# Performance work log

Measured on AMD Instinct MI355X. Metric: run time of the kernel, lower is better.

The kernel has to match this reference:

```python
import jax, jax.numpy as jnp
import numpy as np

SCALING = 32.0 / 16.0  # alpha / r

def setup_inputs() -> dict:
    key = jax.random.key(0)
    k1, k2, k3, k4 = jax.random.split(key, 4)
    B_, S, D_in, D_out, R = 4, 2048, 4096, 4096, 16
    x = jax.random.normal(k1, (B_, S, D_in), dtype=jnp.float32)
    W_base = jax.random.normal(k2, (D_out, D_in), dtype=jnp.float32) * 0.02
    b_base = jax.random.normal(k3, (D_out,), dtype=jnp.float32) * 0.02
    A = jax.random.normal(k4, (R, D_in), dtype=jnp.float32) * 0.02
    B = jnp.zeros((D_out, R), dtype=jnp.float32)  # lora_B init to zeros
    return {"x": x, "W_base": W_base, "b_base": b_base, "A": A, "B": B}

def reference(x, W_base, b_base, A, B):
    # base linear (stands in for dequantized 4-bit matmul): [B,S,Din] @ [Din,Dout]
    out = jnp.einsum('bsd,od->bso', x, W_base) + b_base
    # LoRA path: B(A(x)) * scaling, dropout=0 -> identity
    xa = jnp.einsum('bsd,rd->bsr', x, A)        # [B,S,r]
    delta = jnp.einsum('bsr,or->bso', xa, B)    # [B,S,Dout]
    return out + delta * SCALING
```

## Files before the change

### kernel.cpp

```cpp
#include <hip/hip_runtime.h>


typedef __attribute__((ext_vector_type(4))) float f32x4;
typedef __attribute__((ext_vector_type(8))) short bf16x8;

__device__ __forceinline__ unsigned short f2bf(float f) {
    unsigned u = __builtin_bit_cast(unsigned, f);
    unsigned r = u + 0x7fffu + ((u >> 16) & 1u);
    return (unsigned short)(r >> 16);
}

__device__ __forceinline__ void gload_lds16(const void* g, void* l) {
    __builtin_amdgcn_global_load_lds(
        (const __attribute__((address_space(1))) void*)g,
        (__attribute__((address_space(3))) void*)l, 16, 0, 0);
}

__global__ __launch_bounds__(256) void cast_x_kernel(
    const float* __restrict__ x, unsigned short* __restrict__ xb, int n8)
{
    int stride = gridDim.x * blockDim.x;
    for (int i = blockIdx.x * blockDim.x + threadIdx.x; i < n8; i += stride) {
        size_t base = (size_t)i * 8;
        float4 f0 = *(const float4*)&x[base];
        float4 f1 = *(const float4*)&x[base + 4];
        ushort4 o0, o1;
        o0.x = f2bf(f0.x); o0.y = f2bf(f0.y); o0.z = f2bf(f0.z); o0.w = f2bf(f0.w);
        o1.x = f2bf(f1.x); o1.y = f2bf(f1.y); o1.z = f2bf(f1.z); o1.w = f2bf(f1.w);
        *(ushort4*)&xb[base]     = o0;
        *(ushort4*)&xb[base + 4] = o1;
    }
}

__global__ __launch_bounds__(256) void prep_w_kernel(
    const float* __restrict__ W, const float* __restrict__ A,
    const float* __restrict__ Bl, unsigned short* __restrict__ wb,
    int K, float scale)
{
    __shared__ float Bs[16][16];
    const int t = threadIdx.x;
    const int n0 = blockIdx.y * 16;
    const int k0 = blockIdx.x * 256;
    {
        int nl = t >> 4, r = t & 15;
        Bs[nl][r] = Bl[(size_t)(n0 + nl) * 16 + r];
    }
    __syncthreads();

    const int lane = t & 63;
    const int wv = t >> 6;
    const int k = k0 + lane * 4;

    float4 av[16];
#pragma unroll
    for (int r = 0; r < 16; ++r)
        av[r] = *(const float4*)&A[(size_t)r * K + k];

#pragma unroll
    for (int j = 0; j < 4; ++j) {
        const int nl = wv * 4 + j;
        const int n = n0 + nl;
        float4 w = *(const float4*)&W[(size_t)n * K + k];
        float d0 = 0.f, d1 = 0.f, d2 = 0.f, d3 = 0.f;
#pragma unroll
        for (int r = 0; r < 16; ++r) {
            float b = Bs[nl][r];
            d0 += b * av[r].x; d1 += b * av[r].y;
            d2 += b * av[r].z; d3 += b * av[r].w;
        }
        ushort4 o;
        o.x = f2bf(w.x + scale * d0);
        o.y = f2bf(w.y + scale * d1);
        o.z = f2bf(w.z + scale * d2);
        o.w = f2bf(w.w + scale * d3);
        *(ushort4*)&wb[(size_t)n * K + k] = o;
    }
}


#define SETPRIO(p) __builtin_amdgcn_s_setprio(p)
#define BARRIER()  __builtin_amdgcn_s_barrier()
#define LGKM0()    do { asm volatile("s_waitcnt lgkmcnt(0)" ::: "memory"); \
                        __builtin_amdgcn_sched_barrier(0); } while (0)

__global__ __launch_bounds__(512, 2) void gemm256_kernel(
    const unsigned short* __restrict__ Xb, const unsigned short* __restrict__ Wb,
    const float* __restrict__ bias, float* __restrict__ out,
    int M, int N, int K)
{
    __shared__ __align__(16) unsigned short lds[2][2][2][8192];

    const int NT = K / 64;
    const int ntn = N / 256;
    int bid = blockIdx.x;
    {
        int per = gridDim.x >> 3;
        bid = (bid & 7) * per + (bid >> 3);
    }
    const int tm = bid / ntn, tn = bid % ntn;

    const int t = threadIdx.x;
    const int lane = t & 63, wave = t >> 6;
    const int wr = wave >> 2;
    const int wc = wave & 3;

    const int srow = t >> 3;
    const int scol = ((t & 7) * 8) ^ (((t >> 3) & 7) << 3);
    unsigned gA[2][2], gB[2][2];
#pragma unroll
    for (int h = 0; h < 2; ++h)
#pragma unroll
        for (int i = 0; i < 2; ++i) {
            gA[h][i] = (unsigned)((tm * 256 + h * 128 + i * 64 + srow) * K + scol);
            gB[h][i] = (unsigned)((tn * 256 + h * 128 + i * 64 + srow) * K + scol);
        }

#define ST_A(buf, h, i, kt)                                                     \
    gload_lds16(Xb + gA[h][i] + (kt) * 64,                                      \
                &lds[buf][0][h][(i) * 4096 + wave * 512]);
#define ST_B(buf, h, i, kt)                                                     \
    gload_lds16(Wb + gB[h][i] + (kt) * 64,                                      \
                &lds[buf][1][h][(i) * 4096 + wave * 512]);

    const int fr = lane & 15;
    const int hi16 = ((lane >> 4) & 3) * 16;
    const int bsw = (fr & 7) << 4;
    const int lo0 = hi16 ^ bsw;
    const int lo1 = (64 + hi16) ^ bsw;

    f32x4 acc[8][4] = {};

#pragma unroll
    for (int h = 0; h < 2; ++h)
#pragma unroll
        for (int i = 0; i < 2; ++i) { ST_A(0, h, i, 0) ST_B(0, h, i, 0) }
#pragma unroll
    for (int h = 0; h < 2; ++h)
#pragma unroll
        for (int i = 0; i < 2; ++i) { ST_A(1, h, i, 1) }
    asm volatile("s_waitcnt vmcnt(4)" ::: "memory");
    BARRIER();

#define MFMA_Q(m0, n0)                                                          \
    _Pragma("unroll") for (int mi = m0; mi < m0 + 4; ++mi)                      \
    _Pragma("unroll") for (int ni = n0; ni < n0 + 2; ++ni)                      \
    _Pragma("unroll") for (int kk = 0; kk < 2; ++kk)                            \
        acc[mi][ni] = __builtin_amdgcn_mfma_f32_16x16x32_bf16(                  \
            a[mi][kk], b[ni][kk], acc[mi][ni], 0, 0, 0);

    for (int kt = 0; kt < NT; ++kt) {
        const int cur = kt & 1;
        const char* pA = (const char*)&lds[cur][0][wr][0];
        const char* pB = (const char*)&lds[cur][1][wc >> 1][0];
        const int bro = (wc & 1) * 64;
        const bool stB = (kt + 1 < NT);
        const bool stA = (kt + 2 < NT);

        bf16x8 a[8][2], b[4][2];

#pragma unroll
        for (int mi = 0; mi < 4; ++mi) {
            a[mi][0] = *(const bf16x8*)(pA + (mi * 16 + fr) * 128 + lo0);
            a[mi][1] = *(const bf16x8*)(pA + (mi * 16 + fr) * 128 + lo1);
        }
#pragma unroll
        for (int ni = 0; ni < 2; ++ni) {
            b[ni][0] = *(const bf16x8*)(pB + (bro + ni * 16 + fr) * 128 + lo0);
            b[ni][1] = *(const bf16x8*)(pB + (bro + ni * 16 + fr) * 128 + lo1);
        }
        if (stB) { ST_B(cur ^ 1, 0, 0, kt + 1) ST_B(cur ^ 1, 0, 1, kt + 1) }
        BARRIER();
        LGKM0();
        SETPRIO(1);
        MFMA_Q(0, 0)
        SETPRIO(0);
        BARRIER();

#pragma unroll
        for (int mi = 4; mi < 8; ++mi) {
            a[mi][0] = *(const bf16x8*)(pA + (mi * 16 + fr) * 128 + lo0);
            a[mi][1] = *(const bf16x8*)(pA + (mi * 16 + fr) * 128 + lo1);
        }
        if (stB) { ST_B(cur ^ 1, 1, 0, kt + 1) ST_B(cur ^ 1, 1, 1, kt + 1) }
        BARRIER();
        LGKM0();
        SETPRIO(1);
        MFMA_Q(4, 0)
        SETPRIO(0);
        BARRIER();

#pragma unroll
        for (int ni = 2; ni < 4; ++ni) {
            b[ni][0] = *(const bf16x8*)(pB + (bro + ni * 16 + fr) * 128 + lo0);
            b[ni][1] = *(const bf16x8*)(pB + (bro + ni * 16 + fr) * 128 + lo1);
        }
        if (stA) { ST_A(cur, 0, 0, kt + 2) ST_A(cur, 0, 1, kt + 2) }
        BARRIER();
        LGKM0();
        SETPRIO(1);
        MFMA_Q(0, 2)
        SETPRIO(0);
        BARRIER();

        if (stA) { ST_A(cur, 1, 0, kt + 2) ST_A(cur, 1, 1, kt + 2) }
        BARRIER();
        SETPRIO(1);
        MFMA_Q(4, 2)
        SETPRIO(0);
        if (stA) {
            asm volatile("s_waitcnt vmcnt(4)" ::: "memory");
        } else {
            asm volatile("s_waitcnt vmcnt(0)" ::: "memory");
        }
        BARRIER();
    }

    const int row0 = tm * 256 + wr * 128 + (lane >> 4) * 4;
    const int col0 = tn * 256 + wc * 64;
#pragma unroll
    for (int ni = 0; ni < 4; ++ni) {
        const int col = col0 + ni * 16 + fr;
        const float bv = bias[col];
#pragma unroll
        for (int mi = 0; mi < 8; ++mi) {
            const int row = row0 + mi * 16;
#pragma unroll
            for (int r = 0; r < 4; ++r)
                out[(size_t)(row + r) * N + col] = acc[mi][ni][r] + bv;
        }
    }
}

extern "C" void kernel_launch(void* const* d_in, const int* in_sizes, int n_in,
                              void* d_out, int out_size, void* d_ws, size_t ws_size,
                              hipStream_t stream)
{
    const float* x  = (const float*)d_in[0];
    const float* W  = (const float*)d_in[1];
    const float* b  = (const float*)d_in[2];
    const float* A  = (const float*)d_in[3];
    const float* Bl = (const float*)d_in[4];
    float* out = (float*)d_out;

    const int Dout = in_sizes[2];
    const int Din  = in_sizes[1] / Dout;
    const int M    = in_sizes[0] / Din;

    unsigned short* xb = (unsigned short*)d_ws;
    unsigned short* wb = xb + (size_t)M * Din;

    cast_x_kernel<<<2048, 256, 0, stream>>>(x, xb, M * Din / 8);

    dim3 gw(Din / 256, Dout / 16);
    prep_w_kernel<<<gw, 256, 0, stream>>>(W, A, Bl, wb, Din, 2.0f);

    const int grid = (M / 256) * (Dout / 256);
    gemm256_kernel<<<grid, 512, 0, stream>>>(xb, wb, b, out, M, Dout, Din);
}
```

Before: 306.5 us.

## Restructure GEMM main loop into k-split phases with unrolled double-buffer ticks

The per-tile MFMA schedule now splits work by k-half rather than by n-half. Fragments are loaded in smaller register sets (ak, an, bk), and all four B prefetches are issued in the first phase. The loop is unrolled by two through a templated ktile so the buffer index is a compile-time constant. The sched_barrier inside the lgkmcnt wait is dropped, which gives the compiler more freedom to interleave instructions but may also let it reorder LDS reads in unwanted ways.

After: 509.8 us. +66.4%, slower.

```diff
diff --git a/kernel.cpp b/kernel.cpp
--- a/kernel.cpp
+++ b/kernel.cpp
@@ -80,8 +80,91 @@
 
 #define SETPRIO(p) __builtin_amdgcn_s_setprio(p)
 #define BARRIER()  __builtin_amdgcn_s_barrier()
-#define LGKM0()    do { asm volatile("s_waitcnt lgkmcnt(0)" ::: "memory"); \
-                        __builtin_amdgcn_sched_barrier(0); } while (0)
+#define LGKM0()    asm volatile("s_waitcnt lgkmcnt(0)" ::: "memory")
+
+#define ST_A(buf, h, i, ktt)                                                    \
+    gload_lds16(Xb + gA[h][i] + (ktt) * 64,                                     \
+                &lds[buf][0][h][(i) * 4096 + wave * 512]);
+#define ST_B(buf, h, i, ktt)                                                    \
+    gload_lds16(Wb + gB[h][i] + (ktt) * 64,                                     \
+                &lds[buf][1][h][(i) * 4096 + wave * 512]);
+
+#define MFMA16(ACC_ROW, AV, BV)                                                 \
+    _Pragma("unroll") for (int mi = 0; mi < 4; ++mi)                            \
+    _Pragma("unroll") for (int ni = 0; ni < 4; ++ni)                            \
+        acc[(ACC_ROW) + mi][ni] = __builtin_amdgcn_mfma_f32_16x16x32_bf16(      \
+            AV[mi], BV[ni], acc[(ACC_ROW) + mi][ni], 0, 0, 0);
+
+template<int CUR>
+__device__ __forceinline__ void ktile(
+    int kt, int NT,
+    unsigned short (*lds)[2][2][8192],
+    f32x4 (&acc)[8][4],
+    const unsigned short* __restrict__ Xb, const unsigned short* __restrict__ Wb,
+    const unsigned (&gA)[2][2], const unsigned (&gB)[2][2],
+    int wave, int wr, int wch, int fr, int lo0, int lo1, int bro)
+{
+    const char* pA = (const char*)&lds[CUR][0][wr][0];
+    const char* pB = (const char*)&lds[CUR][1][wch][0];
+    bf16x8 ak[4], an[4], bk[4];
+
+#pragma unroll
+    for (int i = 0; i < 4; ++i)
+        ak[i] = *(const bf16x8*)(pA + (i * 16 + fr) * 128 + lo0);
+#pragma unroll
+    for (int i = 0; i < 4; ++i)
+        bk[i] = *(const bf16x8*)(pB + (bro + i * 16 + fr) * 128 + lo0);
+    if (kt + 1 < NT) {
+        ST_B(CUR ^ 1, 0, 0, kt + 1) ST_B(CUR ^ 1, 0, 1, kt + 1)
+        ST_B(CUR ^ 1, 1, 0, kt + 1) ST_B(CUR ^ 1, 1, 1, kt + 1)
+    }
+    BARRIER();
+    LGKM0();
+    SETPRIO(1);
+    MFMA16(0, ak, bk)
+    SETPRIO(0);
+    BARRIER();
+
+#pragma unroll
+    for (int i = 0; i < 4; ++i)
+        an[i] = *(const bf16x8*)(pA + ((4 + i) * 16 + fr) * 128 + lo0);
+#pragma unroll
+    for (int i = 0; i < 4; ++i)
+        ak[i] = *(const bf16x8*)(pA + (i * 16 + fr) * 128 + lo1);
+    BARRIER();
+    LGKM0();
+    SETPRIO(1);
+    MFMA16(4, an, bk)
+    SETPRIO(0);
+    BARRIER();
+
+#pragma unroll
+    for (int i = 0; i < 4; ++i)
+        an[i] = *(const bf16x8*)(pA + ((4 + i) * 16 + fr) * 128 + lo1);
+#pragma unroll
+    for (int i = 0; i < 4; ++i)
+        bk[i] = *(const bf16x8*)(pB + (bro + i * 16 + fr) * 128 + lo1);
+    BARRIER();
+    LGKM0();
+    SETPRIO(1);
+    MFMA16(0, ak, bk)
+    SETPRIO(0);
+    BARRIER();
+
+    if (kt + 2 < NT) {
+        ST_A(CUR, 0, 0, kt + 2) ST_A(CUR, 0, 1, kt + 2)
+        ST_A(CUR, 1, 0, kt + 2) ST_A(CUR, 1, 1, kt + 2)
+    }
+    SETPRIO(1);
+    MFMA16(4, an, bk)
+    SETPRIO(0);
+    if (kt + 2 < NT) {
+        asm volatile("s_waitcnt vmcnt(4)" ::: "memory");
+    } else {
+        asm volatile("s_waitcnt vmcnt(0)" ::: "memory");
+    }
+    BARRIER();
+}
 
 __global__ __launch_bounds__(512, 2) void gemm256_kernel(
     const unsigned short* __restrict__ Xb, const unsigned short* __restrict__ Wb,
@@ -103,6 +186,8 @@
     const int lane = t & 63, wave = t >> 6;
     const int wr = wave >> 2;
     const int wc = wave & 3;
+    const int wch = wc >> 1;
+    const int bro = (wc & 1) * 64;
 
     const int srow = t >> 3;
     const int scol = ((t & 7) * 8) ^ (((t >> 3) & 7) << 3);
@@ -114,13 +199,6 @@
             gA[h][i] = (unsigned)((tm * 256 + h * 128 + i * 64 + srow) * K + scol);
             gB[h][i] = (unsigned)((tn * 256 + h * 128 + i * 64 + srow) * K + scol);
         }
-
-#define ST_A(buf, h, i, kt)                                                     \
-    gload_lds16(Xb + gA[h][i] + (kt) * 64,                                      \
-                &lds[buf][0][h][(i) * 4096 + wave * 512]);
-#define ST_B(buf, h, i, kt)                                                     \
-    gload_lds16(Wb + gB[h][i] + (kt) * 64,                                      \
-                &lds[buf][1][h][(i) * 4096 + wave * 512]);
 
     const int fr = lane & 15;
     const int hi16 = ((lane >> 4) & 3) * 16;
@@ -141,78 +219,9 @@
     asm volatile("s_waitcnt vmcnt(4)" ::: "memory");
     BARRIER();
 
-#define MFMA_Q(m0, n0)                                                          \
-    _Pragma("unroll") for (int mi = m0; mi < m0 + 4; ++mi)                      \
-    _Pragma("unroll") for (int ni = n0; ni < n0 + 2; ++ni)                      \
-    _Pragma("unroll") for (int kk = 0; kk < 2; ++kk)                            \
-        acc[mi][ni] = __builtin_amdgcn_mfma_f32_16x16x32_bf16(                  \
-            a[mi][kk], b[ni][kk], acc[mi][ni], 0, 0, 0);
-
-    for (int kt = 0; kt < NT; ++kt) {
-        const int cur = kt & 1;
-        const char* pA = (const char*)&lds[cur][0][wr][0];
-        const char* pB = (const char*)&lds[cur][1][wc >> 1][0];
-        const int bro = (wc & 1) * 64;
-        const bool stB = (kt + 1 < NT);
-        const bool stA = (kt + 2 < NT);
-
-        bf16x8 a[8][2], b[4][2];
-
-#pragma unroll
-        for (int mi = 0; mi < 4; ++mi) {
-            a[mi][0] = *(const bf16x8*)(pA + (mi * 16 + fr) * 128 + lo0);
-            a[mi][1] = *(const bf16x8*)(pA + (mi * 16 + fr) * 128 + lo1);
-        }
-#pragma unroll
-        for (int ni = 0; ni < 2; ++ni) {
-            b[ni][0] = *(const bf16x8*)(pB + (bro + ni * 16 + fr) * 128 + lo0);
-            b[ni][1] = *(const bf16x8*)(pB + (bro + ni * 16 + fr) * 128 + lo1);
-        }
-        if (stB) { ST_B(cur ^ 1, 0, 0, kt + 1) ST_B(cur ^ 1, 0, 1, kt + 1) }
-        BARRIER();
-        LGKM0();
-        SETPRIO(1);
-        MFMA_Q(0, 0)
-        SETPRIO(0);
-        BARRIER();
-
-#pragma unroll
-        for (int mi = 4; mi < 8; ++mi) {
-            a[mi][0] = *(const bf16x8*)(pA + (mi * 16 + fr) * 128 + lo0);
-            a[mi][1] = *(const bf16x8*)(pA + (mi * 16 + fr) * 128 + lo1);
-        }
-        if (stB) { ST_B(cur ^ 1, 1, 0, kt + 1) ST_B(cur ^ 1, 1, 1, kt + 1) }
-        BARRIER();
-        LGKM0();
-        SETPRIO(1);
-        MFMA_Q(4, 0)
-        SETPRIO(0);
-        BARRIER();
-
-#pragma unroll
-        for (int ni = 2; ni < 4; ++ni) {
-            b[ni][0] = *(const bf16x8*)(pB + (bro + ni * 16 + fr) * 128 + lo0);
-            b[ni][1] = *(const bf16x8*)(pB + (bro + ni * 16 + fr) * 128 + lo1);
-        }
-        if (stA) { ST_A(cur, 0, 0, kt + 2) ST_A(cur, 0, 1, kt + 2) }
-        BARRIER();
-        LGKM0();
-        SETPRIO(1);
-        MFMA_Q(0, 2)
-        SETPRIO(0);
-        BARRIER();
-
-        if (stA) { ST_A(cur, 1, 0, kt + 2) ST_A(cur, 1, 1, kt + 2) }
-        BARRIER();
-        SETPRIO(1);
-        MFMA_Q(4, 2)
-        SETPRIO(0);
-        if (stA) {
-            asm volatile("s_waitcnt vmcnt(4)" ::: "memory");
-        } else {
-            asm volatile("s_waitcnt vmcnt(0)" ::: "memory");
-        }
-        BARRIER();
+    for (int kt = 0; kt < NT; kt += 2) {
+        ktile<0>(kt,     NT, lds, acc, Xb, Wb, gA, gB, wave, wr, wch, fr, lo0, lo1, bro);
+        ktile<1>(kt + 1, NT, lds, acc, Xb, Wb, gA, gB, wave, wr, wch, fr, lo0, lo1, bro);
     }
 
     const int row0 = tm * 256 + wr * 128 + (lane >> 4) * 4;
```
